# Performance work log

Measured on AMD Instinct MI355X. Metric: run time of the kernel, lower is better.

Reference implementation:

```python
import jax, jax.numpy as jnp
import numpy as np

B, N, C = 8, 1024, 768
H = 12
DH = C // H  # 64
FF = 3072
EPS = 1e-5


def _layer_norm(x, gamma, beta):
    mu = jnp.mean(x, axis=-1, keepdims=True)
    var = jnp.mean(jnp.square(x - mu), axis=-1, keepdims=True)
    return (x - mu) * jax.lax.rsqrt(var + EPS) * gamma + beta


def setup_inputs() -> dict:
    key = jax.random.key(0)
    ks = jax.random.split(key, 16)
    s_in = 1.0 / np.sqrt(C)
    s_ff = 1.0 / np.sqrt(FF)
    return {
        "x": jax.random.normal(ks[0], (B, N, C), dtype=jnp.float32),
        "Wq": jax.random.uniform(ks[1], (C, C), jnp.float32, -s_in, s_in),
        "bq": jax.random.uniform(ks[2], (C,), jnp.float32, -s_in, s_in),
        "Wk": jax.random.uniform(ks[3], (C, C), jnp.float32, -s_in, s_in),
        "bk": jax.random.uniform(ks[4], (C,), jnp.float32, -s_in, s_in),
        "Wv": jax.random.uniform(ks[5], (C, C), jnp.float32, -s_in, s_in),
        "bv": jax.random.uniform(ks[6], (C,), jnp.float32, -s_in, s_in),
        "Wo": jax.random.uniform(ks[7], (C, C), jnp.float32, -s_in, s_in),
        "bo": jax.random.uniform(ks[8], (C,), jnp.float32, -s_in, s_in),
        "g1": jnp.ones((C,), jnp.float32),
        "b1": jnp.zeros((C,), jnp.float32),
        "g2": jnp.ones((C,), jnp.float32),
        "b2": jnp.zeros((C,), jnp.float32),
        "W1": jax.random.uniform(ks[9], (C, FF), jnp.float32, -s_in, s_in),
        "bf1": jax.random.uniform(ks[10], (FF,), jnp.float32, -s_in, s_in),
        "W2": jax.random.uniform(ks[11], (FF, C), jnp.float32, -s_ff, s_ff),
        "bf2": jax.random.uniform(ks[12], (C,), jnp.float32, -s_ff, s_ff),
    }


def reference(x, Wq, bq, Wk, bk, Wv, bv, Wo, bo, g1, b1, g2, b2, W1, bf1, W2, bf2):
    # Pre-norm attention block
    xn = _layer_norm(x, g1, b1)
    q = (xn @ Wq + bq).reshape(B, N, H, DH)
    k = (xn @ Wk + bk).reshape(B, N, H, DH)
    v = (xn @ Wv + bv).reshape(B, N, H, DH)
    scores = jnp.einsum("bqhd,bkhd->bhqk", q, k) / np.sqrt(DH)  # [B,H,N,N]
    attn = jax.nn.softmax(scores, axis=-1)
    z = jnp.einsum("bhqk,bkhd->bqhd", attn, v).reshape(B, N, C)
    attn_out = z @ Wo + bo
    b = x + attn_out  # dropout is identity (p=0 / eval)
    # Pre-norm MLP block
    bn = _layer_norm(b, g2, b2)
    h = jax.nn.relu(bn @ W1 + bf1)
    y = b + (h @ W2 + bf2)
    return y
```

## Files before the change

### kernel.cpp

```cpp
#include <hip/hip_runtime.h>
#include <hip/hip_bf16.h>

#define BDIM 8
#define SEQ  1024
#define CH   768
#define NHD  12
#define DHD  64
#define FFD  3072
#define MR   (BDIM*SEQ)

typedef __attribute__((ext_vector_type(8))) short bf16x8;
typedef __attribute__((ext_vector_type(4))) float f32x4;
typedef unsigned int   u32;
typedef unsigned short u16;

__device__ __forceinline__ u16 f2bfu(float x) {
  __hip_bfloat16 h = __float2bfloat16(x);
  return *reinterpret_cast<u16*>(&h);
}

__device__ __forceinline__ void glds16(const void* g, void* l) {
  __builtin_amdgcn_global_load_lds(
      (const __attribute__((address_space(1))) u32*)g,
      (__attribute__((address_space(3))) u32*)l, 16, 0, 0);
}

__global__ __launch_bounds__(256) void k_transpose_all(
    const float* __restrict__ Wq, const float* __restrict__ Wk,
    const float* __restrict__ Wv, const float* __restrict__ Wo,
    const float* __restrict__ W1, const float* __restrict__ W2,
    u16* __restrict__ ws) {
  __shared__ float tile[32][33];
  int b = blockIdx.x;
  int id, tb;
  if (b < 2304)      { id = b / 576; tb = b % 576; }
  else if (b < 4608) { id = 4;       tb = b - 2304; }
  else               { id = 5;       tb = b - 4608; }
  const float* src;
  u16* dst;
  int K, Nc;
  switch (id) {
    case 0: src = Wq; dst = ws;                      K = CH;  Nc = CH;  break;
    case 1: src = Wk; dst = ws + (size_t)CH*CH;      K = CH;  Nc = CH;  break;
    case 2: src = Wv; dst = ws + (size_t)2*CH*CH;    K = CH;  Nc = CH;  break;
    case 3: src = Wo; dst = ws + (size_t)3*CH*CH;    K = CH;  Nc = CH;  break;
    case 4: src = W1; dst = ws + (size_t)4*CH*CH;    K = CH;  Nc = FFD; break;
    default:src = W2; dst = ws + (size_t)4*CH*CH + (size_t)CH*FFD;
                                                     K = FFD; Nc = CH;  break;
  }
  int tilesx = Nc >> 5;
  int bx = (tb % tilesx) * 32;
  int by = (tb / tilesx) * 32;
  int tx = threadIdx.x & 31, ty = threadIdx.x >> 5;
#pragma unroll
  for (int j = 0; j < 32; j += 8)
    tile[ty + j][tx] = src[(size_t)(by + ty + j) * Nc + bx + tx];
  __syncthreads();
#pragma unroll
  for (int j = 0; j < 32; j += 8)
    dst[(size_t)(bx + ty + j) * K + by + tx] = f2bfu(tile[tx][ty + j]);
}

__global__ __launch_bounds__(256) void k_pack_bias(
    const float* __restrict__ bq, const float* __restrict__ bk,
    const float* __restrict__ bv, float* __restrict__ dst) {
  int i = blockIdx.x * 256 + threadIdx.x;
  if (i < 3 * CH)
    dst[i] = i < CH ? bq[i] : (i < 2 * CH ? bk[i - CH] : bv[i - 2 * CH]);
}

__global__ __launch_bounds__(256) void k_layernorm_bf16(
    const float* __restrict__ src, const float* __restrict__ gamma,
    const float* __restrict__ beta, u16* __restrict__ dst) {
  int row  = blockIdx.x * 4 + (threadIdx.x >> 6);
  int lane = threadIdx.x & 63;
  const float4* p4 = (const float4*)(src + (size_t)row * CH);
  float4 v[3];
  float s = 0.f, s2 = 0.f;
#pragma unroll
  for (int k = 0; k < 3; k++) {
    v[k] = p4[lane + k * 64];
    s  += v[k].x + v[k].y + v[k].z + v[k].w;
    s2 += v[k].x * v[k].x + v[k].y * v[k].y + v[k].z * v[k].z + v[k].w * v[k].w;
  }
#pragma unroll
  for (int m = 1; m < 64; m <<= 1) {
    s  += __shfl_xor(s,  m, 64);
    s2 += __shfl_xor(s2, m, 64);
  }
  float mean = s * (1.f / CH);
  float var  = s2 * (1.f / CH) - mean * mean;
  float rs   = rsqrtf(var + 1e-5f);
  u16* drow = dst + (size_t)row * CH;
#pragma unroll
  for (int k = 0; k < 3; k++) {
    int col = lane * 4 + k * 256;
    float4 gq = ((const float4*)gamma)[lane + k * 64];
    float4 bq = ((const float4*)beta )[lane + k * 64];
    u32 lo = (u32)f2bfu((v[k].x - mean) * rs * gq.x + bq.x) |
             ((u32)f2bfu((v[k].y - mean) * rs * gq.y + bq.y) << 16);
    u32 hi = (u32)f2bfu((v[k].z - mean) * rs * gq.z + bq.z) |
             ((u32)f2bfu((v[k].w - mean) * rs * gq.w + bq.w) << 16);
    uint2 w; w.x = lo; w.y = hi;
    *(uint2*)(drow + col) = w;
  }
}

#define GBN 128
#define GBK 32
enum { EPI_QKV = 0, EPI_RESID = 1, EPI_RELU = 2 };

template <int EPI, int TM = 128>
__global__ __launch_bounds__(256, 2) void k_gemm(
    const u16* __restrict__ A, const u16* __restrict__ Bt,
    const float* __restrict__ bias, const float* __restrict__ resid,
    void* __restrict__ outp, int K, int Nmat) {
  __shared__ u16 As[2][TM * GBK];
  __shared__ u16 Bs[2][GBN * GBK];
  constexpr int MF = TM / 32;
  int tid = threadIdx.x;
  int bm = blockIdx.x, bn = blockIdx.y;
  int lane = tid & 63, wid = tid >> 6;
  int wr = (wid >> 1) * (TM / 2), wc = (wid & 1) * 64;
  int lrow = lane & 15, g = lane >> 4;

  const u16* Abase = A + (size_t)(bm * TM) * K;
  const u16* Bbase = Bt + (size_t)(bn * GBN) * K;
  int srow = tid >> 2;
  int scol = (tid & 3) * 8;

  auto stage = [&](int buf, int k0) {
#pragma unroll
    for (int r = 0; r < TM / 64; r++)
      glds16(Abase + (size_t)(srow + r * 64) * K + k0 + scol,
             &As[buf][(tid + r * 256) * 8]);
#pragma unroll
    for (int r = 0; r < 2; r++)
      glds16(Bbase + (size_t)(srow + r * 64) * K + k0 + scol,
             &Bs[buf][(tid + r * 256) * 8]);
  };

  f32x4 acc[MF][4];
#pragma unroll
  for (int m = 0; m < MF; m++)
#pragma unroll
    for (int n = 0; n < 4; n++) acc[m][n] = {0.f, 0.f, 0.f, 0.f};

  int nk = K / GBK;
  stage(0, 0);
  for (int kt = 0; kt < nk; ++kt) {
    int buf = kt & 1;
    __syncthreads();
    if (kt + 1 < nk) stage(buf ^ 1, (kt + 1) * GBK);
    bf16x8 af[MF], bfr[4];
#pragma unroll
    for (int m = 0; m < MF; m++)
      af[m] = *(const bf16x8*)&As[buf][(wr + m * 16 + lrow) * GBK + g * 8];
#pragma unroll
    for (int n = 0; n < 4; n++)
      bfr[n] = *(const bf16x8*)&Bs[buf][(wc + n * 16 + lrow) * GBK + g * 8];
#pragma unroll
    for (int m = 0; m < MF; m++)
#pragma unroll
      for (int n = 0; n < 4; n++)
        acc[m][n] = __builtin_amdgcn_mfma_f32_16x16x32_bf16(af[m], bfr[n],
                                                            acc[m][n], 0, 0, 0);
  }

#pragma unroll
  for (int m = 0; m < MF; m++) {
    int row0 = bm * TM + wr + m * 16 + g * 4;
#pragma unroll
    for (int n = 0; n < 4; n++) {
      int col = bn * GBN + wc + n * 16 + lrow;
      float bval = bias[col];
      if constexpr (EPI == EPI_QKV) {
        int sel = col / CH;
        int c = col - sel * CH;
        int h = c >> 6, d = c & 63;
        int bb = row0 >> 10, nn0 = row0 & (SEQ - 1);
        if (sel == 2) {
          union { uint2 u; u16 h4[4]; } pk;
#pragma unroll
          for (int r = 0; r < 4; r++) pk.h4[r] = f2bfu(acc[m][n][r] + bval);
          *(uint2*)&((u16*)outp)[(size_t)2 * MR * CH +
                                 (((size_t)(bb * NHD + h)) * DHD + d) * SEQ +
                                 nn0] = pk.u;
        } else {
#pragma unroll
          for (int r = 0; r < 4; r++)
            ((u16*)outp)[(size_t)sel * MR * CH +
                         (((size_t)(bb * NHD + h)) * SEQ + nn0 + r) * DHD + d] =
                f2bfu(acc[m][n][r] + bval);
        }
      } else if constexpr (EPI == EPI_RESID) {
#pragma unroll
        for (int r = 0; r < 4; r++) {
          size_t idx = (size_t)(row0 + r) * Nmat + col;
          ((float*)outp)[idx] = acc[m][n][r] + bval + resid[idx];
        }
      } else {
#pragma unroll
        for (int r = 0; r < 4; r++) {
          float val = acc[m][n][r] + bval;
          ((u16*)outp)[(size_t)(row0 + r) * Nmat + col] =
              f2bfu(val > 0.f ? val : 0.f);
        }
      }
    }
  }
}

__global__ __launch_bounds__(256, 2) void k_attn(
    const u16* __restrict__ Q, const u16* __restrict__ Kk,
    const u16* __restrict__ Vt, u16* __restrict__ Z) {
  __shared__ u16 Ks[2][64 * 64];
  __shared__ u16 Vs[2][64 * 64];
  __shared__ u32 Psu[4][64 * 9];
  int tid = threadIdx.x, lane = tid & 63, wid = tid >> 6;
  int lrow = lane & 15, g = lane >> 4;
  int id  = blockIdx.y * 16 + blockIdx.x;
  int nid = (id & 7) * 192 + (id >> 3);
  int qtile = (nid & 15) * 64;
  int bh = nid >> 4;
  size_t base = (size_t)bh * SEQ * DHD;
  int bb = bh / NHD, hh = bh % NHD;
  int qrow0 = qtile + wid * 16;

  bf16x8 qf[2];
#pragma unroll
  for (int ks = 0; ks < 2; ks++)
    qf[ks] = *(const bf16x8*)(Q + base + (size_t)(qrow0 + lrow) * DHD +
                              ks * 32 + g * 8);

  f32x4 accO[4];
  float mrun = -1e30f, lrun = 0.f;
#pragma unroll
  for (int n = 0; n < 4; n++) accO[n] = {0.f, 0.f, 0.f, 0.f};

  int srow  = tid >> 3;
  int swz   = (((tid & 7) * 16) ^ ((srow & 7) << 4)) >> 1;
  const u16* kg0 = Kk + base + (size_t)srow * DHD + swz;
  const u16* vg0 = Vt + base + (size_t)srow * SEQ + swz;

  auto stageKV = [&](int buf, int t) {
    int kv0 = t * 64;
    const u16* kg = kg0 + (size_t)kv0 * DHD;
    glds16(kg,                    &Ks[buf][tid * 8]);
    glds16(kg + 32 * DHD,         &Ks[buf][2048 + tid * 8]);
    const u16* vg = vg0 + kv0;
    glds16(vg,                    &Vs[buf][tid * 8]);
    glds16(vg + 32 * SEQ,         &Vs[buf][2048 + tid * 8]);
  };

  int rc0 = ((g * 16)      ^ ((lrow & 7) << 4)) >> 1;
  int rc1 = ((64 + g * 16) ^ ((lrow & 7) << 4)) >> 1;

  stageKV(0, 0);
  for (int t = 0; t < 16; ++t) {
    int buf = t & 1;
    __syncthreads();
    if (t + 1 < 16) stageKV(buf ^ 1, t + 1);

    f32x4 sacc[4];
    __builtin_amdgcn_s_setprio(1);
#pragma unroll
    for (int n = 0; n < 4; n++) {
      bf16x8 kf0 = *(const bf16x8*)&Ks[buf][(n * 16 + lrow) * 64 + rc0];
      bf16x8 kf1 = *(const bf16x8*)&Ks[buf][(n * 16 + lrow) * 64 + rc1];
      sacc[n] = {0.f, 0.f, 0.f, 0.f};
      sacc[n] = __builtin_amdgcn_mfma_f32_16x16x32_bf16(kf0, qf[0], sacc[n], 0, 0, 0);
      sacc[n] = __builtin_amdgcn_mfma_f32_16x16x32_bf16(kf1, qf[1], sacc[n], 0, 0, 0);
    }
    __builtin_amdgcn_s_setprio(0);

    float mx = fmaxf(fmaxf(fmaxf(sacc[0][0], sacc[0][1]),
                           fmaxf(sacc[0][2], sacc[0][3])),
                     fmaxf(fmaxf(sacc[1][0], sacc[1][1]),
                           fmaxf(sacc[1][2], sacc[1][3])));
    mx = fmaxf(mx, fmaxf(fmaxf(fmaxf(sacc[2][0], sacc[2][1]),
                               fmaxf(sacc[2][2], sacc[2][3])),
                         fmaxf(fmaxf(sacc[3][0], sacc[3][1]),
                               fmaxf(sacc[3][2], sacc[3][3]))));
    mx *= 0.125f;
    mx = fmaxf(mx, __shfl_xor(mx, 16, 64));
    mx = fmaxf(mx, __shfl_xor(mx, 32, 64));

    if (__all(mx <= mrun + 8.f)) {
      float psum = 0.f;
#pragma unroll
      for (int n = 0; n < 4; n++)
#pragma unroll
        for (int r = 0; r < 4; r++) {
          float p = __expf(sacc[n][r] * 0.125f - mrun);
          sacc[n][r] = p;
          psum += p;
        }
      psum += __shfl_xor(psum, 16, 64);
      psum += __shfl_xor(psum, 32, 64);
      lrun += psum;
    } else {
      float mnew = fmaxf(mrun, mx);
      float alpha = __expf(mrun - mnew);
      float psum = 0.f;
#pragma unroll
      for (int n = 0; n < 4; n++)
#pragma unroll
        for (int r = 0; r < 4; r++) {
          float p = __expf(sacc[n][r] * 0.125f - mnew);
          sacc[n][r] = p;
          psum += p;
        }
      psum += __shfl_xor(psum, 16, 64);
      psum += __shfl_xor(psum, 32, 64);
      lrun = lrun * alpha + psum;
      mrun = mnew;
#pragma unroll
      for (int r = 0; r < 4; r++) {
        float ar = __shfl(alpha, (lane & 48) | (g * 4 + r), 64);
#pragma unroll
        for (int n = 0; n < 4; n++) accO[n][r] *= ar;
      }
    }

#pragma unroll
    for (int n = 0; n < 4; n++) {
      u32 lo = (u32)f2bfu(sacc[n][0]) | ((u32)f2bfu(sacc[n][1]) << 16);
      u32 hi = (u32)f2bfu(sacc[n][2]) | ((u32)f2bfu(sacc[n][3]) << 16);
      Psu[wid][lane * 9 + 2 * n]     = lo;
      Psu[wid][lane * 9 + 2 * n + 1] = hi;
    }

    int laneA = lrow + ((g & 1) << 5);
    int laneB = laneA + 16;
    int nsel = g >> 1;
    __builtin_amdgcn_s_setprio(1);
#pragma unroll
    for (int ks = 0; ks < 2; ks++) {
      int nks = 2 * ks + nsel;
      union { bf16x8 v; u32 w[4]; } pk;
      pk.w[0] = Psu[wid][laneA * 9 + 2 * nks];
      pk.w[1] = Psu[wid][laneA * 9 + 2 * nks + 1];
      pk.w[2] = Psu[wid][laneB * 9 + 2 * nks];
      pk.w[3] = Psu[wid][laneB * 9 + 2 * nks + 1];
      int rc = ks ? rc1 : rc0;
#pragma unroll
      for (int n = 0; n < 4; n++) {
        bf16x8 vf = *(const bf16x8*)&Vs[buf][(n * 16 + lrow) * 64 + rc];
        accO[n] = __builtin_amdgcn_mfma_f32_16x16x32_bf16(pk.v, vf,
                                                          accO[n], 0, 0, 0);
      }
    }
    __builtin_amdgcn_s_setprio(0);
  }

#pragma unroll
  for (int r = 0; r < 4; r++) {
    float lr = __shfl(lrun, (lane & 48) | (g * 4 + r), 64);
    float inv = 1.f / lr;
    int qrow = qrow0 + g * 4 + r;
#pragma unroll
    for (int n = 0; n < 4; n++) {
      int d = n * 16 + lrow;
      Z[((size_t)(bb * SEQ + qrow)) * CH + hh * DHD + d] =
          f2bfu(accO[n][r] * inv);
    }
  }
}

extern "C" void kernel_launch(void* const* d_in, const int* in_sizes, int n_in,
                              void* d_out, int out_size, void* d_ws,
                              size_t ws_size, hipStream_t stream) {
  (void)in_sizes; (void)n_in; (void)out_size; (void)ws_size;
  const float* x   = (const float*)d_in[0];
  const float* Wq  = (const float*)d_in[1];
  const float* bq  = (const float*)d_in[2];
  const float* Wk  = (const float*)d_in[3];
  const float* bk  = (const float*)d_in[4];
  const float* Wv  = (const float*)d_in[5];
  const float* bv  = (const float*)d_in[6];
  const float* Wo  = (const float*)d_in[7];
  const float* bo  = (const float*)d_in[8];
  const float* g1  = (const float*)d_in[9];
  const float* b1  = (const float*)d_in[10];
  const float* g2  = (const float*)d_in[11];
  const float* b2  = (const float*)d_in[12];
  const float* W1  = (const float*)d_in[13];
  const float* bf1 = (const float*)d_in[14];
  const float* W2  = (const float*)d_in[15];
  const float* bf2 = (const float*)d_in[16];

  u16* wsu  = (u16*)d_ws;
  u16* wq_t = wsu;
  u16* wo_t = wq_t + (size_t)3 * CH * CH;
  u16* w1_t = wo_t + (size_t)CH * CH;
  u16* w2_t = w1_t + (size_t)CH * FFD;
  u16* xn   = w2_t + (size_t)CH * FFD;
  u16* qb   = xn + (size_t)MR * CH;
  u16* zb   = qb + (size_t)3 * MR * CH;
  float* bres = (float*)(zb + (size_t)MR * CH);
  u16* hb   = qb;
  float* bqkv = (float*)d_out;

  dim3 blk(256);
  k_transpose_all<<<6912, blk, 0, stream>>>(Wq, Wk, Wv, Wo, W1, W2, wsu);
  k_pack_bias<<<9, blk, 0, stream>>>(bq, bk, bv, bqkv);

  k_layernorm_bf16<<<2048, blk, 0, stream>>>(x, g1, b1, xn);
  k_gemm<EPI_QKV><<<dim3(64, 18), blk, 0, stream>>>(xn, wq_t, bqkv, nullptr,
                                                    qb, CH, 3 * CH);
  k_attn<<<dim3(16, 96), blk, 0, stream>>>(qb, qb + (size_t)MR * CH,
                                           qb + (size_t)2 * MR * CH, zb);
  k_gemm<EPI_RESID, 64><<<dim3(128, 6), blk, 0, stream>>>(zb, wo_t, bo, x,
                                                          bres, CH, CH);
  k_layernorm_bf16<<<2048, blk, 0, stream>>>(bres, g2, b2, xn);
  k_gemm<EPI_RELU><<<dim3(64, 24), blk, 0, stream>>>(xn, w1_t, bf1, nullptr,
                                                     hb, CH, FFD);
  k_gemm<EPI_RESID, 64><<<dim3(128, 6), blk, 0, stream>>>(hb, w2_t, bf2, bres,
                                                          (float*)d_out, FFD, CH);
}
```

Baseline: 263.5 us.

## Swizzle GEMM LDS tiles, add MFMA priority, widen attention blocks to 128 queries

The GEMM now XOR-swizzles the 16-byte k-chunks it writes to LDS and reads them back with the same swizzle, aiming to remove LDS bank conflicts on the fragment loads. It also raises wave priority around the MFMA loop. The attention kernel moves to 512-thread blocks with 8 waves covering 128 query rows, so each staged K/V tile is reused by twice as many waves and each thread issues half the loads. The epilogue is pulled out into a helper function. Larger attention blocks can lower occupancy, and the launch-bounds change (512, 4) puts pressure on register allocation.

```diff
diff --git a/kernel.cpp b/kernel.cpp
--- a/kernel.cpp
+++ b/kernel.cpp
@@ -106,17 +106,54 @@
   }
 }
 
-#define GBN 128
-#define GBK 32
 enum { EPI_QKV = 0, EPI_RESID = 1, EPI_RELU = 2 };
+
+template <int EPI>
+__device__ __forceinline__ void gemm_epi(const f32x4& a, int row0, int col,
+                                         float bval, const float* resid,
+                                         void* outp, int Nmat) {
+  if constexpr (EPI == EPI_QKV) {
+    int sel = col / CH;
+    int c = col - sel * CH;
+    int h = c >> 6, d = c & 63;
+    int bb = row0 >> 10, nn0 = row0 & (SEQ - 1);
+    if (sel == 2) {
+      union { uint2 u; u16 h4[4]; } pk;
+#pragma unroll
+      for (int r = 0; r < 4; r++) pk.h4[r] = f2bfu(a[r] + bval);
+      *(uint2*)&((u16*)outp)[(size_t)2 * MR * CH +
+                             (((size_t)(bb * NHD + h)) * DHD + d) * SEQ + nn0] =
+          pk.u;
+    } else {
+#pragma unroll
+      for (int r = 0; r < 4; r++)
+        ((u16*)outp)[(size_t)sel * MR * CH +
+                     (((size_t)(bb * NHD + h)) * SEQ + nn0 + r) * DHD + d] =
+            f2bfu(a[r] + bval);
+    }
+  } else if constexpr (EPI == EPI_RESID) {
+#pragma unroll
+    for (int r = 0; r < 4; r++) {
+      size_t idx = (size_t)(row0 + r) * Nmat + col;
+      ((float*)outp)[idx] = a[r] + bval + resid[idx];
+    }
+  } else {
+#pragma unroll
+    for (int r = 0; r < 4; r++) {
+      float val = a[r] + bval;
+      ((u16*)outp)[(size_t)(row0 + r) * Nmat + col] =
+          f2bfu(val > 0.f ? val : 0.f);
+    }
+  }
+}
 
 template <int EPI, int TM = 128>
 __global__ __launch_bounds__(256, 2) void k_gemm(
     const u16* __restrict__ A, const u16* __restrict__ Bt,
     const float* __restrict__ bias, const float* __restrict__ resid,
     void* __restrict__ outp, int K, int Nmat) {
-  __shared__ u16 As[2][TM * GBK];
-  __shared__ u16 Bs[2][GBN * GBK];
+  __shared__ u16 As[2][TM * 32];
+  __shared__ u16 Bs[2][128 * 32];
   constexpr int MF = TM / 32;
   int tid = threadIdx.x;
   int bm = blockIdx.x, bn = blockIdx.y;
@@ -125,46 +162,54 @@
   int lrow = lane & 15, g = lane >> 4;
 
   const u16* Abase = A + (size_t)(bm * TM) * K;
-  const u16* Bbase = Bt + (size_t)(bn * GBN) * K;
-  int srow = tid >> 2;
-  int scol = (tid & 3) * 8;
+  const u16* Bbase = Bt + (size_t)(bn * 128) * K;
 
   auto stage = [&](int buf, int k0) {
 #pragma unroll
-    for (int r = 0; r < TM / 64; r++)
-      glds16(Abase + (size_t)(srow + r * 64) * K + k0 + scol,
-             &As[buf][(tid + r * 256) * 8]);
-#pragma unroll
-    for (int r = 0; r < 2; r++)
-      glds16(Bbase + (size_t)(srow + r * 64) * K + k0 + scol,
-             &Bs[buf][(tid + r * 256) * 8]);
+    for (int r = 0; r < TM / 64; r++) {
+      int c = tid + r * 256;
+      int row = c >> 2;
+      int scol = ((c & 3) ^ ((row >> 1) & 3)) * 8;
+      glds16(Abase + (size_t)row * K + k0 + scol, &As[buf][c * 8]);
+    }
+#pragma unroll
+    for (int r = 0; r < 2; r++) {
+      int c = tid + r * 256;
+      int row = c >> 2;
+      int scol = ((c & 3) ^ ((row >> 1) & 3)) * 8;
+      glds16(Bbase + (size_t)row * K + k0 + scol, &Bs[buf][c * 8]);
+    }
   };
 
+  int xsl = (g ^ ((lrow >> 1) & 3)) * 8;
+
   f32x4 acc[MF][4];
 #pragma unroll
   for (int m = 0; m < MF; m++)
 #pragma unroll
     for (int n = 0; n < 4; n++) acc[m][n] = {0.f, 0.f, 0.f, 0.f};
 
-  int nk = K / GBK;
+  int nk = K >> 5;
   stage(0, 0);
   for (int kt = 0; kt < nk; ++kt) {
     int buf = kt & 1;
     __syncthreads();
-    if (kt + 1 < nk) stage(buf ^ 1, (kt + 1) * GBK);
+    if (kt + 1 < nk) stage(buf ^ 1, (kt + 1) << 5);
     bf16x8 af[MF], bfr[4];
 #pragma unroll
     for (int m = 0; m < MF; m++)
-      af[m] = *(const bf16x8*)&As[buf][(wr + m * 16 + lrow) * GBK + g * 8];
+      af[m] = *(const bf16x8*)&As[buf][(wr + m * 16 + lrow) * 32 + xsl];
 #pragma unroll
     for (int n = 0; n < 4; n++)
-      bfr[n] = *(const bf16x8*)&Bs[buf][(wc + n * 16 + lrow) * GBK + g * 8];
+      bfr[n] = *(const bf16x8*)&Bs[buf][(wc + n * 16 + lrow) * 32 + xsl];
+    __builtin_amdgcn_s_setprio(1);
 #pragma unroll
     for (int m = 0; m < MF; m++)
 #pragma unroll
       for (int n = 0; n < 4; n++)
         acc[m][n] = __builtin_amdgcn_mfma_f32_16x16x32_bf16(af[m], bfr[n],
                                                             acc[m][n], 0, 0, 0);
+    __builtin_amdgcn_s_setprio(0);
   }
 
 #pragma unroll
@@ -172,57 +217,24 @@
     int row0 = bm * TM + wr + m * 16 + g * 4;
 #pragma unroll
     for (int n = 0; n < 4; n++) {
-      int col = bn * GBN + wc + n * 16 + lrow;
-      float bval = bias[col];
-      if constexpr (EPI == EPI_QKV) {
-        int sel = col / CH;
-        int c = col - sel * CH;
-        int h = c >> 6, d = c & 63;
-        int bb = row0 >> 10, nn0 = row0 & (SEQ - 1);
-        if (sel == 2) {
-          union { uint2 u; u16 h4[4]; } pk;
-#pragma unroll
-          for (int r = 0; r < 4; r++) pk.h4[r] = f2bfu(acc[m][n][r] + bval);
-          *(uint2*)&((u16*)outp)[(size_t)2 * MR * CH +
-                                 (((size_t)(bb * NHD + h)) * DHD + d) * SEQ +
-                                 nn0] = pk.u;
-        } else {
-#pragma unroll
-          for (int r = 0; r < 4; r++)
-            ((u16*)outp)[(size_t)sel * MR * CH +
-                         (((size_t)(bb * NHD + h)) * SEQ + nn0 + r) * DHD + d] =
-                f2bfu(acc[m][n][r] + bval);
-        }
-      } else if constexpr (EPI == EPI_RESID) {
-#pragma unroll
-        for (int r = 0; r < 4; r++) {
-          size_t idx = (size_t)(row0 + r) * Nmat + col;
-          ((float*)outp)[idx] = acc[m][n][r] + bval + resid[idx];
-        }
-      } else {
-#pragma unroll
-        for (int r = 0; r < 4; r++) {
-          float val = acc[m][n][r] + bval;
-          ((u16*)outp)[(size_t)(row0 + r) * Nmat + col] =
-              f2bfu(val > 0.f ? val : 0.f);
-        }
-      }
-    }
-  }
-}
-
-__global__ __launch_bounds__(256, 2) void k_attn(
+      int col = bn * 128 + wc + n * 16 + lrow;
+      gemm_epi<EPI>(acc[m][n], row0, col, bias[col], resid, outp, Nmat);
+    }
+  }
+}
+
+__global__ __launch_bounds__(512, 4) void k_attn(
     const u16* __restrict__ Q, const u16* __restrict__ Kk,
     const u16* __restrict__ Vt, u16* __restrict__ Z) {
   __shared__ u16 Ks[2][64 * 64];
   __shared__ u16 Vs[2][64 * 64];
-  __shared__ u32 Psu[4][64 * 9];
+  __shared__ u32 Psu[8][64 * 9];
   int tid = threadIdx.x, lane = tid & 63, wid = tid >> 6;
   int lrow = lane & 15, g = lane >> 4;
-  int id  = blockIdx.y * 16 + blockIdx.x;
-  int nid = (id & 7) * 192 + (id >> 3);
-  int qtile = (nid & 15) * 64;
-  int bh = nid >> 4;
+  int id  = blockIdx.x;
+  int nid = (id & 7) * 96 + (id >> 3);
+  int bh = nid >> 3;
+  int qtile = (nid & 7) * 128;
   size_t base = (size_t)bh * SEQ * DHD;
   int bb = bh / NHD, hh = bh % NHD;
   int qrow0 = qtile + wid * 16;
@@ -238,19 +250,14 @@
 #pragma unroll
   for (int n = 0; n < 4; n++) accO[n] = {0.f, 0.f, 0.f, 0.f};
 
-  int srow  = tid >> 3;
-  int swz   = (((tid & 7) * 16) ^ ((srow & 7) << 4)) >> 1;
+  int srow = tid >> 3;
+  int swz  = (((tid & 7) * 16) ^ ((srow & 7) << 4)) >> 1;
   const u16* kg0 = Kk + base + (size_t)srow * DHD + swz;
   const u16* vg0 = Vt + base + (size_t)srow * SEQ + swz;
 
   auto stageKV = [&](int buf, int t) {
-    int kv0 = t * 64;
-    const u16* kg = kg0 + (size_t)kv0 * DHD;
-    glds16(kg,                    &Ks[buf][tid * 8]);
-    glds16(kg + 32 * DHD,         &Ks[buf][2048 + tid * 8]);
-    const u16* vg = vg0 + kv0;
-    glds16(vg,                    &Vs[buf][tid * 8]);
-    glds16(vg + 32 * SEQ,         &Vs[buf][2048 + tid * 8]);
+    glds16(kg0 + (size_t)t * 64 * DHD, &Ks[buf][tid * 8]);
+    glds16(vg0 + t * 64,               &Vs[buf][tid * 8]);
   };
 
   int rc0 = ((g * 16)      ^ ((lrow & 7) << 4)) >> 1;
@@ -407,15 +414,15 @@
   k_pack_bias<<<9, blk, 0, stream>>>(bq, bk, bv, bqkv);
 
   k_layernorm_bf16<<<2048, blk, 0, stream>>>(x, g1, b1, xn);
-  k_gemm<EPI_QKV><<<dim3(64, 18), blk, 0, stream>>>(xn, wq_t, bqkv, nullptr,
-                                                    qb, CH, 3 * CH);
-  k_attn<<<dim3(16, 96), blk, 0, stream>>>(qb, qb + (size_t)MR * CH,
-                                           qb + (size_t)2 * MR * CH, zb);
-  k_gemm<EPI_RESID, 64><<<dim3(128, 6), blk, 0, stream>>>(zb, wo_t, bo, x,
-                                                          bres, CH, CH);
+  k_gemm<EPI_QKV, 128><<<dim3(64, 18), blk, 0, stream>>>(
+      xn, wq_t, bqkv, nullptr, qb, CH, 3 * CH);
+  k_attn<<<768, dim3(512), 0, stream>>>(qb, qb + (size_t)MR * CH,
+                                        qb + (size_t)2 * MR * CH, zb);
+  k_gemm<EPI_RESID, 64><<<dim3(128, 6), blk, 0, stream>>>(
+      zb, wo_t, bo, x, bres, CH, CH);
   k_layernorm_bf16<<<2048, blk, 0, stream>>>(bres, g2, b2, xn);
-  k_gemm<EPI_RELU><<<dim3(64, 24), blk, 0, stream>>>(xn, w1_t, bf1, nullptr,
-                                                     hb, CH, FFD);
-  k_gemm<EPI_RESID, 64><<<dim3(128, 6), blk, 0, stream>>>(hb, w2_t, bf2, bres,
-                                                          (float*)d_out, FFD, CH);
-}
+  k_gemm<EPI_RELU, 128><<<dim3(64, 24), blk, 0, stream>>>(
+      xn, w1_t, bf1, nullptr, hb, CH, FFD);
+  k_gemm<EPI_RESID, 64><<<dim3(128, 6), blk, 0, stream>>>(
+      hb, w2_t, bf2, bres, (float*)d_out, FFD, CH);
+}
```

Result: no change. 262.1 us (-0.5%).
